# Performance work log

Measured on AMD Instinct MI355X. Metric: run time of the kernel, lower is better.

The kernel has to match this reference:

```python
import jax, jax.numpy as jnp
import numpy as np

C_IN, C_HID, N_HEADS = 128, 32, 4
INF = 1.0e9
LN_EPS = 1e-5


def setup_inputs() -> dict:
    key = jax.random.key(0)
    ks = jax.random.split(key, 12)
    B, I, J, C, H, D = 1, 384, 384, C_IN, N_HEADS, C_HID
    s = 0.02
    return {
        "x": jax.random.normal(ks[0], (B, I, J, C), dtype=jnp.float32),
        "mask": jnp.ones((B, I, J), dtype=jnp.float32),
        "ln_g": jnp.ones((C,), dtype=jnp.float32),
        "ln_b": jnp.zeros((C,), dtype=jnp.float32),
        "w_tri": jax.random.normal(ks[1], (C, H), dtype=jnp.float32) * s,
        "wq": jax.random.normal(ks[2], (C, H, D), dtype=jnp.float32) * s,
        "wk": jax.random.normal(ks[3], (C, H, D), dtype=jnp.float32) * s,
        "wv": jax.random.normal(ks[4], (C, H, D), dtype=jnp.float32) * s,
        "wg": jax.random.normal(ks[5], (C, H, D), dtype=jnp.float32) * s,
        "bg": jnp.ones((H, D), dtype=jnp.float32),
        "wo": jax.random.normal(ks[6], (H, D, C), dtype=jnp.float32) * s,
        "bo": jnp.zeros((C,), dtype=jnp.float32),
    }


def reference(x, mask, ln_g, ln_b, w_tri, wq, wk, wv, wg, bg, wo, bo):
    # LayerNorm over channel dim
    mu = jnp.mean(x, axis=-1, keepdims=True)
    var = jnp.mean(jnp.square(x - mu), axis=-1, keepdims=True)
    xn = (x - mu) * jax.lax.rsqrt(var + LN_EPS) * ln_g + ln_b  # [B,I,J,C]

    # mask bias: [B, I, 1, 1, J]
    mask_bias = (INF * (mask - 1.0))[..., :, None, None, :]
    # triangle bias: linear(x) -> [B,I,J,H] -> [B,1,H,I,J]
    tri_bias = jnp.einsum("bijc,ch->bhij", xn, w_tri)[:, None]

    scale = 1.0 / jnp.sqrt(jnp.asarray(C_HID, dtype=xn.dtype))
    # per-row attention over J: tensors [B, I, H, J, D]
    q = jnp.einsum("bixc,chd->bihxd", xn, wq) * scale
    k = jnp.einsum("bixc,chd->bihxd", xn, wk)
    v = jnp.einsum("bixc,chd->bihxd", xn, wv)

    logits = jnp.einsum("bihqd,bihkd->bihqk", q, k) + mask_bias + tri_bias
    a = jax.nn.softmax(logits, axis=-1)
    o = jnp.einsum("bihqk,bihkd->bihqd", a, v)  # [B,I,H,J,D]

    g = jax.nn.sigmoid(jnp.einsum("bixc,chd->bihxd", xn, wg) + bg[None, None, :, None, :])
    o = o * g
    out = jnp.einsum("bihxd,hdc->bixc", o, wo) + bo  # [B,I,J,C]
    return out
```

## Files before the change

kernel.cpp:

```cpp
#include <hip/hip_runtime.h>
#include <math.h>


#define I_DIM 384
#define J_DIM 384
#define C_DIM 128
#define H_DIM 4
#define D_DIM 32
#define NPOS (I_DIM * J_DIM)
#define Q_SCALE 0.17677669529663687f

typedef __attribute__((ext_vector_type(8))) short bf16x8;
typedef __attribute__((ext_vector_type(4))) float f32x4;

__device__ __forceinline__ float sigmoidf_(float v) {
    return 1.0f / (1.0f + __expf(-v));
}
__device__ __forceinline__ unsigned short f2bf(float f) {
    union { float f; unsigned u; } x; x.f = f;
    unsigned u = x.u;
    u += 0x7fffu + ((u >> 16) & 1u);
    return (unsigned short)(u >> 16);
}
__device__ __forceinline__ float bf2f(unsigned short v) {
    union { unsigned u; float f; } x; x.u = ((unsigned)v) << 16;
    return x.f;
}

__global__ __launch_bounds__(256) void prep_kernel(
    const float* __restrict__ wq, const float* __restrict__ wk,
    const float* __restrict__ wv, const float* __restrict__ wg,
    const float* __restrict__ wo, unsigned short* __restrict__ Wt)
{
    const int mat = blockIdx.x;
    const float* W = (mat == 0) ? wq : (mat == 1) ? wk : (mat == 2) ? wv
                    : (mat == 3) ? wg : wo;
    const float scale = (mat == 0) ? Q_SCALE : 1.0f;
    const int t = threadIdx.x;
    const int n = t >> 1, c0 = (t & 1) * 64;
#pragma unroll
    for (int u = 0; u < 8; ++u) {
        unsigned pk[4];
#pragma unroll
        for (int w = 0; w < 4; ++w) {
            const unsigned short a = f2bf(W[(size_t)(c0 + u * 8 + w * 2 + 0) * 128 + n] * scale);
            const unsigned short b = f2bf(W[(size_t)(c0 + u * 8 + w * 2 + 1) * 128 + n] * scale);
            pk[w] = (unsigned)a | ((unsigned)b << 16);
        }
        int4 q; q.x = pk[0]; q.y = pk[1]; q.z = pk[2]; q.w = pk[3];
        *(int4*)(Wt + (size_t)mat * 16384 + n * 128 + c0 + u * 8) = q;
    }
}

__global__ __launch_bounds__(256, 4) void proj_kernel(
    const float* __restrict__ x, const float* __restrict__ ln_g,
    const float* __restrict__ ln_b, const float* __restrict__ w_tri,
    const unsigned short* __restrict__ Wt, const float* __restrict__ bg,
    unsigned short* __restrict__ qb, unsigned short* __restrict__ kb,
    unsigned short* __restrict__ vb, unsigned short* __restrict__ gb,
    float* __restrict__ tri)
{
    __shared__ unsigned short At[128 * 128];
    __shared__ unsigned short Ct[128 * 32];

    const int t = threadIdx.x;
    const int pos0 = blockIdx.x * 128;
    const int lane = t & 63, wave = t >> 6;
    const int q15 = lane & 15, quad = lane >> 4;

    {
        const int g = t >> 2, q = t & 3;
#pragma unroll
        for (int rr = 0; rr < 2; ++rr) {
            const int r = g * 2 + rr;
            const float* xrow = x + (size_t)(pos0 + r) * C_DIM + q * 32;
            float xv[32];
            float s = 0.f, ss = 0.f;
#pragma unroll
            for (int u = 0; u < 8; ++u) {
                float4 v4 = ((const float4*)xrow)[u];
                xv[u * 4 + 0] = v4.x; xv[u * 4 + 1] = v4.y;
                xv[u * 4 + 2] = v4.z; xv[u * 4 + 3] = v4.w;
                s  += v4.x + v4.y + v4.z + v4.w;
                ss += v4.x * v4.x + v4.y * v4.y + v4.z * v4.z + v4.w * v4.w;
            }
            s  += __shfl_xor(s, 1);  s  += __shfl_xor(s, 2);
            ss += __shfl_xor(ss, 1); ss += __shfl_xor(ss, 2);
            const float mu  = s * (1.0f / 128.0f);
            const float var = ss * (1.0f / 128.0f) - mu * mu;
            const float rstd = rsqrtf(var + 1e-5f);

            float ptri[4] = {0.f, 0.f, 0.f, 0.f};
#pragma unroll
            for (int u2 = 0; u2 < 4; ++u2) {
                const int cb = q * 32 + u2 * 8;
                const float4 g0 = *(const float4*)(ln_g + cb);
                const float4 g1 = *(const float4*)(ln_g + cb + 4);
                const float4 b0 = *(const float4*)(ln_b + cb);
                const float4 b1 = *(const float4*)(ln_b + cb + 4);
                float xn8[8];
                xn8[0] = (xv[u2 * 8 + 0] - mu) * rstd * g0.x + b0.x;
                xn8[1] = (xv[u2 * 8 + 1] - mu) * rstd * g0.y + b0.y;
                xn8[2] = (xv[u2 * 8 + 2] - mu) * rstd * g0.z + b0.z;
                xn8[3] = (xv[u2 * 8 + 3] - mu) * rstd * g0.w + b0.w;
                xn8[4] = (xv[u2 * 8 + 4] - mu) * rstd * g1.x + b1.x;
                xn8[5] = (xv[u2 * 8 + 5] - mu) * rstd * g1.y + b1.y;
                xn8[6] = (xv[u2 * 8 + 6] - mu) * rstd * g1.z + b1.z;
                xn8[7] = (xv[u2 * 8 + 7] - mu) * rstd * g1.w + b1.w;
#pragma unroll
                for (int w = 0; w < 8; ++w) {
                    const float4 wt = ((const float4*)w_tri)[cb + w];
                    ptri[0] += xn8[w] * wt.x; ptri[1] += xn8[w] * wt.y;
                    ptri[2] += xn8[w] * wt.z; ptri[3] += xn8[w] * wt.w;
                }
                unsigned pk[4];
#pragma unroll
                for (int w = 0; w < 4; ++w)
                    pk[w] = (unsigned)f2bf(xn8[w * 2]) | ((unsigned)f2bf(xn8[w * 2 + 1]) << 16);
                int4 q4; q4.x = pk[0]; q4.y = pk[1]; q4.z = pk[2]; q4.w = pk[3];
                const int c = q * 4 + u2;
                *(int4*)&At[r * 128 + ((c ^ (r & 7)) * 8)] = q4;
            }
#pragma unroll
            for (int hh = 0; hh < 4; ++hh) {
                ptri[hh] += __shfl_xor(ptri[hh], 1);
                ptri[hh] += __shfl_xor(ptri[hh], 2);
            }
            const int pos = pos0 + r;
            const int i = pos / J_DIM, j = pos - (pos / J_DIM) * J_DIM;
            tri[((size_t)q * J_DIM + j) * I_DIM + i] = ptri[q];
        }
    }
    __syncthreads();

    const int m0 = wave * 32;
    for (int mat = 0; mat < 4; ++mat) {
        const unsigned short* WtM = Wt + (size_t)mat * 16384;

        f32x4 acc[2][8];
#pragma unroll
        for (int mt = 0; mt < 2; ++mt)
#pragma unroll
            for (int nt = 0; nt < 8; ++nt) acc[mt][nt] = (f32x4){0.f, 0.f, 0.f, 0.f};

#pragma unroll
        for (int kk = 0; kk < 4; ++kk) {
            const int sw = ((kk * 4 + quad) ^ (q15 & 7)) * 8;
            const bf16x8 a0 = *(const bf16x8*)&At[(m0 + q15) * 128 + sw];
            const bf16x8 a1 = *(const bf16x8*)&At[(m0 + 16 + q15) * 128 + sw];
            const unsigned short* bp = WtM + q15 * 128 + (kk * 4 + quad) * 8;
#pragma unroll
            for (int nt = 0; nt < 8; ++nt) {
                const bf16x8 b = *(const bf16x8*)(bp + nt * 16 * 128);
                acc[0][nt] = __builtin_amdgcn_mfma_f32_16x16x32_bf16(a0, b, acc[0][nt], 0, 0, 0);
                acc[1][nt] = __builtin_amdgcn_mfma_f32_16x16x32_bf16(a1, b, acc[1][nt], 0, 0, 0);
            }
        }

        unsigned short* O = (mat == 0) ? qb : (mat == 1) ? kb : (mat == 2) ? vb : gb;
#pragma unroll
        for (int qp = 0; qp < 4; ++qp) {
            __syncthreads();
#pragma unroll
            for (int mt = 0; mt < 2; ++mt)
#pragma unroll
                for (int n2 = 0; n2 < 2; ++n2) {
                    const int nt = qp * 2 + n2;
                    const int lc = n2 * 16 + q15;
                    const float bgl = (mat == 3) ? bg[qp * 32 + lc] : 0.f;
#pragma unroll
                    for (int reg = 0; reg < 4; ++reg) {
                        float v = acc[mt][nt][reg];
                        if (mat == 3) v = sigmoidf_(v + bgl);
                        const int row = m0 + mt * 16 + quad * 4 + reg;
                        const int cs = ((lc >> 3) ^ (row & 3) ^ ((row >> 2) & 3)) & 3;
                        Ct[row * 32 + cs * 8 + (lc & 7)] = f2bf(v);
                    }
                }
            __syncthreads();
#pragma unroll
            for (int s = 0; s < 2; ++s) {
                const int ch = s * 256 + t;
                const int r = ch >> 2, c = ch & 3;
                const int cs = (c ^ (r & 3) ^ ((r >> 2) & 3)) & 3;
                const int4 v = *(const int4*)&Ct[r * 32 + cs * 8];
                const int pos = pos0 + r;
                const int i = pos / J_DIM, j = pos - (pos / J_DIM) * J_DIM;
                *(int4*)(O + (((size_t)i * H_DIM + qp) * J_DIM + j) * D_DIM + c * 8) = v;
            }
        }
    }
}

__global__ __launch_bounds__(256) void attn_kernel(
    const unsigned short* __restrict__ qb, const unsigned short* __restrict__ kb,
    const unsigned short* __restrict__ vb, unsigned short* gob,
    const float* __restrict__ triT, const float* __restrict__ mask)
{
    __shared__ unsigned short Klds[64 * 32];
    __shared__ unsigned short Vt[32 * 68];
    __shared__ unsigned short Plds[4][32 * 68];
    __shared__ float Mb[J_DIM];

    const int t = threadIdx.x;
    const int lane = t & 63, wave = t >> 6;
    const int q15 = lane & 15, quad = lane >> 4;
    const int i = blockIdx.x >> 2, h = blockIdx.x & 3;
    const size_t hb = (size_t)(i * H_DIM + h) * (J_DIM * D_DIM);
    const int m0 = wave * 96;

    for (int idx = t; idx < J_DIM; idx += 256)
        Mb[idx] = 1.0e9f * (mask[i * J_DIM + idx] - 1.0f);

    bf16x8 qf[6];
#pragma unroll
    for (int m = 0; m < 6; ++m)
        qf[m] = *(const bf16x8*)(qb + hb + (size_t)(m0 + m * 16 + q15) * D_DIM + quad * 8);

    f32x4 Oacc[6][2];
    float sums[6][4];
#pragma unroll
    for (int m = 0; m < 6; ++m) {
#pragma unroll
        for (int d2 = 0; d2 < 2; ++d2) Oacc[m][d2] = (f32x4){0.f, 0.f, 0.f, 0.f};
#pragma unroll
        for (int r = 0; r < 4; ++r) sums[m][r] = 0.f;
    }

    unsigned short* Pw = Plds[wave];
    const float* triH = triT + (size_t)h * J_DIM * I_DIM;

    for (int kt = 0; kt < 6; ++kt) {
        __syncthreads();
        {
            const int kp = t >> 2, du = (t & 3) * 8;
            const size_t gsrc = hb + (size_t)(kt * 64 + kp) * D_DIM + du;
            *(int4*)&Klds[kp * 32 + du] = *(const int4*)(kb + gsrc);
            int4 vv = *(const int4*)(vb + gsrc);
            const unsigned short* vs = (const unsigned short*)&vv;
#pragma unroll
            for (int u = 0; u < 8; ++u)
                Vt[(du + u) * 68 + kp] = vs[u];
        }
        __syncthreads();

        bf16x8 vf[2][2];
#pragma unroll
        for (int ks = 0; ks < 2; ++ks)
#pragma unroll
            for (int d2 = 0; d2 < 2; ++d2)
                vf[ks][d2] = *(const bf16x8*)&Vt[(d2 * 16 + q15) * 68 + ks * 32 + quad * 8];

#pragma unroll
        for (int pass = 0; pass < 3; ++pass) {
            const int mbase = pass * 2;

#pragma unroll
            for (int nt = 0; nt < 4; ++nt) {
                const bf16x8 kf = *(const bf16x8*)&Klds[(nt * 16 + q15) * 32 + quad * 8];
                const float mb = Mb[kt * 64 + nt * 16 + q15];
                const float* tcol = triH + (size_t)(kt * 64 + nt * 16 + q15) * I_DIM;
#pragma unroll
                for (int mm = 0; mm < 2; ++mm) {
                    const int m = mbase + mm;
                    const float4 tb = *(const float4*)(tcol + m0 + m * 16 + quad * 4);
                    f32x4 s = {0.f, 0.f, 0.f, 0.f};
                    s = __builtin_amdgcn_mfma_f32_16x16x32_bf16(qf[m], kf, s, 0, 0, 0);
                    const float p0 = __expf(s[0] + mb + tb.x);
                    const float p1 = __expf(s[1] + mb + tb.y);
                    const float p2 = __expf(s[2] + mb + tb.z);
                    const float p3 = __expf(s[3] + mb + tb.w);
                    sums[m][0] += p0; sums[m][1] += p1;
                    sums[m][2] += p2; sums[m][3] += p3;
                    const int row = mm * 16 + quad * 4;
                    const int col = nt * 16 + q15;
                    Pw[(row + 0) * 68 + col] = f2bf(p0);
                    Pw[(row + 1) * 68 + col] = f2bf(p1);
                    Pw[(row + 2) * 68 + col] = f2bf(p2);
                    Pw[(row + 3) * 68 + col] = f2bf(p3);
                }
            }

#pragma unroll
            for (int mm = 0; mm < 2; ++mm) {
                const int m = mbase + mm;
#pragma unroll
                for (int ks = 0; ks < 2; ++ks) {
                    const bf16x8 af = *(const bf16x8*)&Pw[(mm * 16 + q15) * 68 + ks * 32 + quad * 8];
                    Oacc[m][0] = __builtin_amdgcn_mfma_f32_16x16x32_bf16(af, vf[ks][0], Oacc[m][0], 0, 0, 0);
                    Oacc[m][1] = __builtin_amdgcn_mfma_f32_16x16x32_bf16(af, vf[ks][1], Oacc[m][1], 0, 0, 0);
                }
            }
        }
    }

    float inv[6][4];
#pragma unroll
    for (int m = 0; m < 6; ++m)
#pragma unroll
        for (int r = 0; r < 4; ++r) {
            float s0 = sums[m][r];
            s0 += __shfl_xor(s0, 1); s0 += __shfl_xor(s0, 2);
            s0 += __shfl_xor(s0, 4); s0 += __shfl_xor(s0, 8);
            inv[m][r] = 1.0f / s0;
        }

#pragma unroll
    for (int m = 0; m < 6; ++m) {
        const int qrow = m0 + m * 16 + quad * 4;
#pragma unroll
        for (int d2 = 0; d2 < 2; ++d2) {
            const int d = d2 * 16 + q15;
#pragma unroll
            for (int r = 0; r < 4; ++r) {
                const size_t idx = hb + (size_t)(qrow + r) * D_DIM + d;
                const float g = bf2f(gob[idx]);
                gob[idx] = f2bf(Oacc[m][d2][r] * inv[m][r] * g);
            }
        }
    }
}

__global__ __launch_bounds__(256, 4) void out_kernel(
    const unsigned short* __restrict__ og, const unsigned short* __restrict__ WtO,
    const float* __restrict__ bo, float* __restrict__ out)
{
    __shared__ unsigned short At[128 * 128];

    const int t = threadIdx.x;
    const int pos0 = blockIdx.x * 128;
    const int lane = t & 63, wave = t >> 6;
    const int q15 = lane & 15, quad = lane >> 4;

    {
        const int r = t >> 1, half = t & 1;
        const int pos = pos0 + r;
        const int i = pos / J_DIM, j = pos - (pos / J_DIM) * J_DIM;
#pragma unroll
        for (int u = 0; u < 8; ++u) {
            const int k0 = half * 64 + u * 8;
            const int hh = k0 >> 5, d0 = k0 & 31;
            const int4 v = *(const int4*)(og + (((size_t)i * H_DIM + hh) * J_DIM + j) * D_DIM + d0);
            const int c = half * 8 + u;
            *(int4*)&At[r * 128 + ((c ^ (r & 7)) * 8)] = v;
        }
    }
    __syncthreads();

    const int m0 = wave * 32;
    f32x4 acc[2][8];
#pragma unroll
    for (int mt = 0; mt < 2; ++mt)
#pragma unroll
        for (int nt = 0; nt < 8; ++nt) acc[mt][nt] = (f32x4){0.f, 0.f, 0.f, 0.f};

#pragma unroll
    for (int kk = 0; kk < 4; ++kk) {
        const int sw = ((kk * 4 + quad) ^ (q15 & 7)) * 8;
        const bf16x8 a0 = *(const bf16x8*)&At[(m0 + q15) * 128 + sw];
        const bf16x8 a1 = *(const bf16x8*)&At[(m0 + 16 + q15) * 128 + sw];
        const unsigned short* bp = WtO + q15 * 128 + (kk * 4 + quad) * 8;
#pragma unroll
        for (int nt = 0; nt < 8; ++nt) {
            const bf16x8 b = *(const bf16x8*)(bp + nt * 16 * 128);
            acc[0][nt] = __builtin_amdgcn_mfma_f32_16x16x32_bf16(a0, b, acc[0][nt], 0, 0, 0);
            acc[1][nt] = __builtin_amdgcn_mfma_f32_16x16x32_bf16(a1, b, acc[1][nt], 0, 0, 0);
        }
    }

#pragma unroll
    for (int mt = 0; mt < 2; ++mt)
#pragma unroll
        for (int nt = 0; nt < 8; ++nt) {
            const float bov = bo[nt * 16 + q15];
#pragma unroll
            for (int reg = 0; reg < 4; ++reg) {
                const int pos = pos0 + m0 + mt * 16 + quad * 4 + reg;
                out[(size_t)pos * C_DIM + nt * 16 + q15] = acc[mt][nt][reg] + bov;
            }
        }
}

extern "C" void kernel_launch(void* const* d_in, const int* in_sizes, int n_in,
                              void* d_out, int out_size, void* d_ws, size_t ws_size,
                              hipStream_t stream)
{
    const float* x     = (const float*)d_in[0];
    const float* mask  = (const float*)d_in[1];
    const float* ln_g  = (const float*)d_in[2];
    const float* ln_b  = (const float*)d_in[3];
    const float* w_tri = (const float*)d_in[4];
    const float* wq    = (const float*)d_in[5];
    const float* wk    = (const float*)d_in[6];
    const float* wv    = (const float*)d_in[7];
    const float* wg    = (const float*)d_in[8];
    const float* bg    = (const float*)d_in[9];
    const float* wo    = (const float*)d_in[10];
    const float* bo    = (const float*)d_in[11];
    float* out = (float*)d_out;
    char* ws = (char*)d_ws;

    const size_t NE = (size_t)NPOS * 128;
    unsigned short* qb = (unsigned short*)ws;
    unsigned short* kb = (unsigned short*)(ws + NE * 2);
    unsigned short* vb = (unsigned short*)(ws + NE * 4);
    unsigned short* gb = (unsigned short*)(ws + NE * 6);
    float*         tri = (float*)(ws + NE * 8);
    unsigned short* Wt = (unsigned short*)(ws + NE * 8 + (size_t)NPOS * 4 * 4);

    prep_kernel<<<5, 256, 0, stream>>>(wq, wk, wv, wg, wo, Wt);
    proj_kernel<<<NPOS / 128, 256, 0, stream>>>(x, ln_g, ln_b, w_tri, Wt, bg,
                                                qb, kb, vb, gb, tri);
    attn_kernel<<<I_DIM * H_DIM, 256, 0, stream>>>(qb, kb, vb, gb, tri, mask);
    out_kernel<<<NPOS / 128, 256, 0, stream>>>(gb, Wt + 4 * 16384, bo, out);
}
```

Baseline: 537.8 us.

## Coalesce tri writes with separate transpose, widen proj epilogue, stage WtO in LDS

The projection kernel now writes the triangle bias in row-major [h][i][j] order, giving coalesced stores instead of strided transposed ones. A new in-place tile-transpose kernel then restores the [h][j][i] layout that attention expects. The proj epilogue stages the full 128-column tile in a larger LDS buffer with one sync pair per matrix instead of four, and out_kernel loads the output weight matrix into swizzled LDS rather than reading it from global memory per MFMA. The cost is an extra kernel launch and another pass over tri, plus more LDS per block (and occupancy hints removed), which may cut occupancy.

Result: slower. 564.5 us (+5.0%).

```diff
diff --git a/kernel.cpp b/kernel.cpp
--- a/kernel.cpp
+++ b/kernel.cpp
@@ -52,7 +52,7 @@
     }
 }
 
-__global__ __launch_bounds__(256, 4) void proj_kernel(
+__global__ __launch_bounds__(256) void proj_kernel(
     const float* __restrict__ x, const float* __restrict__ ln_g,
     const float* __restrict__ ln_b, const float* __restrict__ w_tri,
     const unsigned short* __restrict__ Wt, const float* __restrict__ bg,
@@ -61,7 +61,7 @@
     float* __restrict__ tri)
 {
     __shared__ unsigned short At[128 * 128];
-    __shared__ unsigned short Ct[128 * 32];
+    __shared__ unsigned short Ct[128 * 128];
 
     const int t = threadIdx.x;
     const int pos0 = blockIdx.x * 128;
@@ -128,7 +128,7 @@
             }
             const int pos = pos0 + r;
             const int i = pos / J_DIM, j = pos - (pos / J_DIM) * J_DIM;
-            tri[((size_t)q * J_DIM + j) * I_DIM + i] = ptri[q];
+            tri[((size_t)q * I_DIM + i) * J_DIM + j] = ptri[q];
         }
     }
     __syncthreads();
@@ -157,38 +157,70 @@
             }
         }
 
-        unsigned short* O = (mat == 0) ? qb : (mat == 1) ? kb : (mat == 2) ? vb : gb;
-#pragma unroll
-        for (int qp = 0; qp < 4; ++qp) {
-            __syncthreads();
-#pragma unroll
-            for (int mt = 0; mt < 2; ++mt)
-#pragma unroll
-                for (int n2 = 0; n2 < 2; ++n2) {
-                    const int nt = qp * 2 + n2;
-                    const int lc = n2 * 16 + q15;
-                    const float bgl = (mat == 3) ? bg[qp * 32 + lc] : 0.f;
-#pragma unroll
-                    for (int reg = 0; reg < 4; ++reg) {
-                        float v = acc[mt][nt][reg];
-                        if (mat == 3) v = sigmoidf_(v + bgl);
-                        const int row = m0 + mt * 16 + quad * 4 + reg;
-                        const int cs = ((lc >> 3) ^ (row & 3) ^ ((row >> 2) & 3)) & 3;
-                        Ct[row * 32 + cs * 8 + (lc & 7)] = f2bf(v);
-                    }
+        __syncthreads();
+#pragma unroll
+        for (int mt = 0; mt < 2; ++mt)
+#pragma unroll
+            for (int nt = 0; nt < 8; ++nt) {
+                const int col = nt * 16 + q15;
+                const float bgl = (mat == 3) ? bg[col] : 0.f;
+#pragma unroll
+                for (int reg = 0; reg < 4; ++reg) {
+                    float v = acc[mt][nt][reg];
+                    if (mat == 3) v = sigmoidf_(v + bgl);
+                    const int row = m0 + mt * 16 + quad * 4 + reg;
+                    Ct[row * 128 + (((col >> 3) ^ (row & 7)) * 8) + (col & 7)] = f2bf(v);
                 }
-            __syncthreads();
-#pragma unroll
-            for (int s = 0; s < 2; ++s) {
-                const int ch = s * 256 + t;
-                const int r = ch >> 2, c = ch & 3;
-                const int cs = (c ^ (r & 3) ^ ((r >> 2) & 3)) & 3;
-                const int4 v = *(const int4*)&Ct[r * 32 + cs * 8];
+            }
+        __syncthreads();
+        {
+            unsigned short* O = (mat == 0) ? qb : (mat == 1) ? kb : (mat == 2) ? vb : gb;
+#pragma unroll
+            for (int sgm = 0; sgm < 2; ++sgm) {
+                const int ch = t + sgm * 256;
+                const int r = ch >> 2, hh = ch & 3;
                 const int pos = pos0 + r;
                 const int i = pos / J_DIM, j = pos - (pos / J_DIM) * J_DIM;
-                *(int4*)(O + (((size_t)i * H_DIM + qp) * J_DIM + j) * D_DIM + c * 8) = v;
-            }
-        }
+                unsigned short* dst = O + (((size_t)i * H_DIM + hh) * J_DIM + j) * D_DIM;
+#pragma unroll
+                for (int w = 0; w < 4; ++w) {
+                    const int c = hh * 4 + w;
+                    *(int4*)(dst + w * 8) = *(const int4*)&Ct[r * 128 + ((c ^ (r & 7)) * 8)];
+                }
+            }
+        }
+    }
+}
+
+__global__ __launch_bounds__(256) void tri_tr_kernel(float* __restrict__ tri)
+{
+    const int h = blockIdx.x / 78;
+    int rem = blockIdx.x - h * 78;
+    int ti = 0;
+    while (rem >= 12 - ti) { rem -= 12 - ti; ++ti; }
+    const int tj = ti + rem;
+
+    float* T = tri + (size_t)h * I_DIM * J_DIM;
+    __shared__ float A[32][33];
+    __shared__ float B[32][33];
+
+    const int t = threadIdx.x;
+    const int r = t >> 3, c4 = (t & 7) * 4;
+
+    {
+        const float4 v = *(const float4*)(T + (size_t)(ti * 32 + r) * J_DIM + tj * 32 + c4);
+        A[r][c4 + 0] = v.x; A[r][c4 + 1] = v.y; A[r][c4 + 2] = v.z; A[r][c4 + 3] = v.w;
+        const float4 w = *(const float4*)(T + (size_t)(tj * 32 + r) * J_DIM + ti * 32 + c4);
+        B[r][c4 + 0] = w.x; B[r][c4 + 1] = w.y; B[r][c4 + 2] = w.z; B[r][c4 + 3] = w.w;
+    }
+    __syncthreads();
+    {
+        float4 v;
+        v.x = B[c4 + 0][r]; v.y = B[c4 + 1][r]; v.z = B[c4 + 2][r]; v.w = B[c4 + 3][r];
+        *(float4*)(T + (size_t)(ti * 32 + r) * J_DIM + tj * 32 + c4) = v;
+        float4 w;
+        w.x = A[c4 + 0][r]; w.y = A[c4 + 1][r]; w.z = A[c4 + 2][r]; w.w = A[c4 + 3][r];
+        *(float4*)(T + (size_t)(tj * 32 + r) * J_DIM + ti * 32 + c4) = w;
     }
 }
 
@@ -321,11 +353,12 @@
     }
 }
 
-__global__ __launch_bounds__(256, 4) void out_kernel(
+__global__ __launch_bounds__(256) void out_kernel(
     const unsigned short* __restrict__ og, const unsigned short* __restrict__ WtO,
     const float* __restrict__ bo, float* __restrict__ out)
 {
     __shared__ unsigned short At[128 * 128];
+    __shared__ unsigned short Bt[128 * 128];
 
     const int t = threadIdx.x;
     const int pos0 = blockIdx.x * 128;
@@ -344,6 +377,12 @@
             const int c = half * 8 + u;
             *(int4*)&At[r * 128 + ((c ^ (r & 7)) * 8)] = v;
         }
+        const unsigned short* src = WtO + r * 128 + half * 64;
+#pragma unroll
+        for (int u = 0; u < 8; ++u) {
+            const int c = half * 8 + u;
+            *(int4*)&Bt[r * 128 + ((c ^ (r & 7)) * 8)] = *(const int4*)(src + u * 8);
+        }
     }
     __syncthreads();
 
@@ -359,10 +398,9 @@
         const int sw = ((kk * 4 + quad) ^ (q15 & 7)) * 8;
         const bf16x8 a0 = *(const bf16x8*)&At[(m0 + q15) * 128 + sw];
         const bf16x8 a1 = *(const bf16x8*)&At[(m0 + 16 + q15) * 128 + sw];
-        const unsigned short* bp = WtO + q15 * 128 + (kk * 4 + quad) * 8;
 #pragma unroll
         for (int nt = 0; nt < 8; ++nt) {
-            const bf16x8 b = *(const bf16x8*)(bp + nt * 16 * 128);
+            const bf16x8 b = *(const bf16x8*)&Bt[(nt * 16 + q15) * 128 + sw];
             acc[0][nt] = __builtin_amdgcn_mfma_f32_16x16x32_bf16(a0, b, acc[0][nt], 0, 0, 0);
             acc[1][nt] = __builtin_amdgcn_mfma_f32_16x16x32_bf16(a1, b, acc[1][nt], 0, 0, 0);
         }
@@ -411,6 +449,7 @@
     prep_kernel<<<5, 256, 0, stream>>>(wq, wk, wv, wg, wo, Wt);
     proj_kernel<<<NPOS / 128, 256, 0, stream>>>(x, ln_g, ln_b, w_tri, Wt, bg,
                                                 qb, kb, vb, gb, tri);
+    tri_tr_kernel<<<H_DIM * 78, 256, 0, stream>>>(tri);
     attn_kernel<<<I_DIM * H_DIM, 256, 0, stream>>>(qb, kb, vb, gb, tri, mask);
     out_kernel<<<NPOS / 128, 256, 0, stream>>>(gb, Wt + 4 * 16384, bo, out);
 }
```

## Fuse attention with output projection; write tri bias coalesced then transpose in place

Applied to the files above, without the earlier changes.

The attention and output-projection kernels are merged. Each block handles one row i and half of the queries, with one wave per head. The gated attention output is staged in LDS and multiplied by Wo directly, so the intermediate gated tensor is no longer written to and read back from global memory. The projection kernel now stores the triangle bias in coalesced [h,i,j] order, and a new in-place 32x32 tile transpose kernel converts it to the [h,j,i] layout the attention kernel expects. In exchange, each wave loads its own K/V tiles (more LDS and more global traffic per block), there are fewer blocks per head, and the output GEMM is split unevenly across waves.

After: 756.6 us. +40.7%, slower.

```diff
diff --git a/kernel.cpp b/kernel.cpp
--- a/kernel.cpp
+++ b/kernel.cpp
@@ -128,7 +128,7 @@
             }
             const int pos = pos0 + r;
             const int i = pos / J_DIM, j = pos - (pos / J_DIM) * J_DIM;
-            tri[((size_t)q * J_DIM + j) * I_DIM + i] = ptri[q];
+            tri[((size_t)q * I_DIM + i) * J_DIM + j] = ptri[q];
         }
     }
     __syncthreads();
@@ -192,193 +192,222 @@
     }
 }
 
-__global__ __launch_bounds__(256) void attn_kernel(
+__global__ __launch_bounds__(256) void tri_tr_kernel(float* __restrict__ tri)
+{
+    const int h = blockIdx.x / 78;
+    int rem = blockIdx.x - h * 78;
+    int ti = 0;
+    while (rem >= 12 - ti) { rem -= 12 - ti; ++ti; }
+    const int tj = ti + rem;
+
+    float* T = tri + (size_t)h * I_DIM * J_DIM;
+    __shared__ float A[32][33];
+    __shared__ float B[32][33];
+
+    const int t = threadIdx.x;
+    const int r = t >> 3, c4 = (t & 7) * 4;
+
+    {
+        const float4 v = *(const float4*)(T + (size_t)(ti * 32 + r) * J_DIM + tj * 32 + c4);
+        A[r][c4 + 0] = v.x; A[r][c4 + 1] = v.y; A[r][c4 + 2] = v.z; A[r][c4 + 3] = v.w;
+        const float4 w = *(const float4*)(T + (size_t)(tj * 32 + r) * J_DIM + ti * 32 + c4);
+        B[r][c4 + 0] = w.x; B[r][c4 + 1] = w.y; B[r][c4 + 2] = w.z; B[r][c4 + 3] = w.w;
+    }
+    __syncthreads();
+    {
+        float4 v;
+        v.x = B[c4 + 0][r]; v.y = B[c4 + 1][r]; v.z = B[c4 + 2][r]; v.w = B[c4 + 3][r];
+        *(float4*)(T + (size_t)(ti * 32 + r) * J_DIM + tj * 32 + c4) = v;
+        float4 w;
+        w.x = A[c4 + 0][r]; w.y = A[c4 + 1][r]; w.z = A[c4 + 2][r]; w.w = A[c4 + 3][r];
+        *(float4*)(T + (size_t)(tj * 32 + r) * J_DIM + ti * 32 + c4) = w;
+    }
+}
+
+struct SmemKVP {
+    unsigned short K[4][64 * 32];
+    unsigned short V[4][32 * 68];
+    unsigned short P[4][32 * 68];
+};
+union SmemU {
+    SmemKVP a;
+    unsigned short og[96 * 128];
+};
+
+__global__ __launch_bounds__(256, 3) void attn_out_kernel(
     const unsigned short* __restrict__ qb, const unsigned short* __restrict__ kb,
-    const unsigned short* __restrict__ vb, unsigned short* gob,
-    const float* __restrict__ triT, const float* __restrict__ mask)
+    const unsigned short* __restrict__ vb, const unsigned short* __restrict__ gb,
+    const float* __restrict__ triT, const float* __restrict__ mask,
+    const unsigned short* __restrict__ WtO, const float* __restrict__ bo,
+    float* __restrict__ out)
 {
-    __shared__ unsigned short Klds[64 * 32];
-    __shared__ unsigned short Vt[32 * 68];
-    __shared__ unsigned short Plds[4][32 * 68];
+    __shared__ SmemU sm;
     __shared__ float Mb[J_DIM];
 
     const int t = threadIdx.x;
     const int lane = t & 63, wave = t >> 6;
     const int q15 = lane & 15, quad = lane >> 4;
-    const int i = blockIdx.x >> 2, h = blockIdx.x & 3;
+    const int i = blockIdx.x >> 1, half = blockIdx.x & 1;
+    const int h = wave;
     const size_t hb = (size_t)(i * H_DIM + h) * (J_DIM * D_DIM);
-    const int m0 = wave * 96;
+    const float* triH = triT + (size_t)h * J_DIM * I_DIM;
 
     for (int idx = t; idx < J_DIM; idx += 256)
         Mb[idx] = 1.0e9f * (mask[i * J_DIM + idx] - 1.0f);
 
-    bf16x8 qf[6];
-#pragma unroll
-    for (int m = 0; m < 6; ++m)
-        qf[m] = *(const bf16x8*)(qb + hb + (size_t)(m0 + m * 16 + q15) * D_DIM + quad * 8);
-
-    f32x4 Oacc[6][2];
-    float sums[6][4];
-#pragma unroll
-    for (int m = 0; m < 6; ++m) {
-#pragma unroll
-        for (int d2 = 0; d2 < 2; ++d2) Oacc[m][d2] = (f32x4){0.f, 0.f, 0.f, 0.f};
-#pragma unroll
-        for (int r = 0; r < 4; ++r) sums[m][r] = 0.f;
-    }
-
-    unsigned short* Pw = Plds[wave];
-    const float* triH = triT + (size_t)h * J_DIM * I_DIM;
-
-    for (int kt = 0; kt < 6; ++kt) {
+    unsigned short* Kw = sm.a.K[wave];
+    unsigned short* Vw = sm.a.V[wave];
+    unsigned short* Pw = sm.a.P[wave];
+
+    for (int sub = 0; sub < 2; ++sub) {
+        const int q0 = half * 192 + sub * 96;
         __syncthreads();
-        {
-            const int kp = t >> 2, du = (t & 3) * 8;
-            const size_t gsrc = hb + (size_t)(kt * 64 + kp) * D_DIM + du;
-            *(int4*)&Klds[kp * 32 + du] = *(const int4*)(kb + gsrc);
-            int4 vv = *(const int4*)(vb + gsrc);
-            const unsigned short* vs = (const unsigned short*)&vv;
-#pragma unroll
-            for (int u = 0; u < 8; ++u)
-                Vt[(du + u) * 68 + kp] = vs[u];
-        }
-        __syncthreads();
-
-        bf16x8 vf[2][2];
-#pragma unroll
-        for (int ks = 0; ks < 2; ++ks)
-#pragma unroll
-            for (int d2 = 0; d2 < 2; ++d2)
-                vf[ks][d2] = *(const bf16x8*)&Vt[(d2 * 16 + q15) * 68 + ks * 32 + quad * 8];
-
-#pragma unroll
-        for (int pass = 0; pass < 3; ++pass) {
-            const int mbase = pass * 2;
-
-#pragma unroll
-            for (int nt = 0; nt < 4; ++nt) {
-                const bf16x8 kf = *(const bf16x8*)&Klds[(nt * 16 + q15) * 32 + quad * 8];
-                const float mb = Mb[kt * 64 + nt * 16 + q15];
-                const float* tcol = triH + (size_t)(kt * 64 + nt * 16 + q15) * I_DIM;
+
+        bf16x8 qf[6];
+#pragma unroll
+        for (int m = 0; m < 6; ++m)
+            qf[m] = *(const bf16x8*)(qb + hb + (size_t)(q0 + m * 16 + q15) * D_DIM + quad * 8);
+
+        f32x4 Oacc[6][2];
+        float sums[6][4];
+#pragma unroll
+        for (int m = 0; m < 6; ++m) {
+#pragma unroll
+            for (int d2 = 0; d2 < 2; ++d2) Oacc[m][d2] = (f32x4){0.f, 0.f, 0.f, 0.f};
+#pragma unroll
+            for (int r = 0; r < 4; ++r) sums[m][r] = 0.f;
+        }
+
+        for (int kt = 0; kt < 6; ++kt) {
+            {
+                const size_t gsrc = hb + (size_t)(kt * 64 + lane) * D_DIM;
+                int4 k0 = *(const int4*)(kb + gsrc);
+                int4 k1 = *(const int4*)(kb + gsrc + 8);
+                int4 k2 = *(const int4*)(kb + gsrc + 16);
+                int4 k3 = *(const int4*)(kb + gsrc + 24);
+                *(int4*)&Kw[lane * 32 + 0]  = k0;
+                *(int4*)&Kw[lane * 32 + 8]  = k1;
+                *(int4*)&Kw[lane * 32 + 16] = k2;
+                *(int4*)&Kw[lane * 32 + 24] = k3;
+                int4 vv[4];
+                vv[0] = *(const int4*)(vb + gsrc);
+                vv[1] = *(const int4*)(vb + gsrc + 8);
+                vv[2] = *(const int4*)(vb + gsrc + 16);
+                vv[3] = *(const int4*)(vb + gsrc + 24);
+#pragma unroll
+                for (int p = 0; p < 4; ++p) {
+                    const unsigned short* vs = (const unsigned short*)&vv[p];
+#pragma unroll
+                    for (int u = 0; u < 8; ++u)
+                        Vw[(p * 8 + u) * 68 + lane] = vs[u];
+                }
+            }
+
+            bf16x8 vf[2][2];
+#pragma unroll
+            for (int ks = 0; ks < 2; ++ks)
+#pragma unroll
+                for (int d2 = 0; d2 < 2; ++d2)
+                    vf[ks][d2] = *(const bf16x8*)&Vw[(d2 * 16 + q15) * 68 + ks * 32 + quad * 8];
+
+#pragma unroll
+            for (int pass = 0; pass < 3; ++pass) {
+                const int mbase = pass * 2;
+#pragma unroll
+                for (int nt = 0; nt < 4; ++nt) {
+                    const bf16x8 kf = *(const bf16x8*)&Kw[(nt * 16 + q15) * 32 + quad * 8];
+                    const float mb = Mb[kt * 64 + nt * 16 + q15];
+                    const float* tcol = triH + (size_t)(kt * 64 + nt * 16 + q15) * I_DIM;
+#pragma unroll
+                    for (int mm = 0; mm < 2; ++mm) {
+                        const int m = mbase + mm;
+                        const float4 tb = *(const float4*)(tcol + q0 + m * 16 + quad * 4);
+                        f32x4 s = {0.f, 0.f, 0.f, 0.f};
+                        s = __builtin_amdgcn_mfma_f32_16x16x32_bf16(qf[m], kf, s, 0, 0, 0);
+                        const float p0 = __expf(s[0] + mb + tb.x);
+                        const float p1 = __expf(s[1] + mb + tb.y);
+                        const float p2 = __expf(s[2] + mb + tb.z);
+                        const float p3 = __expf(s[3] + mb + tb.w);
+                        sums[m][0] += p0; sums[m][1] += p1;
+                        sums[m][2] += p2; sums[m][3] += p3;
+                        const int row = mm * 16 + quad * 4;
+                        const int col = nt * 16 + q15;
+                        Pw[(row + 0) * 68 + col] = f2bf(p0);
+                        Pw[(row + 1) * 68 + col] = f2bf(p1);
+                        Pw[(row + 2) * 68 + col] = f2bf(p2);
+                        Pw[(row + 3) * 68 + col] = f2bf(p3);
+                    }
+                }
 #pragma unroll
                 for (int mm = 0; mm < 2; ++mm) {
                     const int m = mbase + mm;
-                    const float4 tb = *(const float4*)(tcol + m0 + m * 16 + quad * 4);
-                    f32x4 s = {0.f, 0.f, 0.f, 0.f};
-                    s = __builtin_amdgcn_mfma_f32_16x16x32_bf16(qf[m], kf, s, 0, 0, 0);
-                    const float p0 = __expf(s[0] + mb + tb.x);
-                    const float p1 = __expf(s[1] + mb + tb.y);
-                    const float p2 = __expf(s[2] + mb + tb.z);
-                    const float p3 = __expf(s[3] + mb + tb.w);
-                    sums[m][0] += p0; sums[m][1] += p1;
-                    sums[m][2] += p2; sums[m][3] += p3;
-                    const int row = mm * 16 + quad * 4;
-                    const int col = nt * 16 + q15;
-                    Pw[(row + 0) * 68 + col] = f2bf(p0);
-                    Pw[(row + 1) * 68 + col] = f2bf(p1);
-                    Pw[(row + 2) * 68 + col] = f2bf(p2);
-                    Pw[(row + 3) * 68 + col] = f2bf(p3);
-                }
-            }
-
-#pragma unroll
-            for (int mm = 0; mm < 2; ++mm) {
-                const int m = mbase + mm;
-#pragma unroll
-                for (int ks = 0; ks < 2; ++ks) {
-                    const bf16x8 af = *(const bf16x8*)&Pw[(mm * 16 + q15) * 68 + ks * 32 + quad * 8];
-                    Oacc[m][0] = __builtin_amdgcn_mfma_f32_16x16x32_bf16(af, vf[ks][0], Oacc[m][0], 0, 0, 0);
-                    Oacc[m][1] = __builtin_amdgcn_mfma_f32_16x16x32_bf16(af, vf[ks][1], Oacc[m][1], 0, 0, 0);
-                }
-            }
-        }
-    }
-
-    float inv[6][4];
-#pragma unroll
-    for (int m = 0; m < 6; ++m)
-#pragma unroll
-        for (int r = 0; r < 4; ++r) {
-            float s0 = sums[m][r];
-            s0 += __shfl_xor(s0, 1); s0 += __shfl_xor(s0, 2);
-            s0 += __shfl_xor(s0, 4); s0 += __shfl_xor(s0, 8);
-            inv[m][r] = 1.0f / s0;
-        }
-
-#pragma unroll
-    for (int m = 0; m < 6; ++m) {
-        const int qrow = m0 + m * 16 + quad * 4;
-#pragma unroll
-        for (int d2 = 0; d2 < 2; ++d2) {
-            const int d = d2 * 16 + q15;
+#pragma unroll
+                    for (int ks = 0; ks < 2; ++ks) {
+                        const bf16x8 af = *(const bf16x8*)&Pw[(mm * 16 + q15) * 68 + ks * 32 + quad * 8];
+                        Oacc[m][0] = __builtin_amdgcn_mfma_f32_16x16x32_bf16(af, vf[ks][0], Oacc[m][0], 0, 0, 0);
+                        Oacc[m][1] = __builtin_amdgcn_mfma_f32_16x16x32_bf16(af, vf[ks][1], Oacc[m][1], 0, 0, 0);
+                    }
+                }
+            }
+        }
+
+        float inv[6][4];
+#pragma unroll
+        for (int m = 0; m < 6; ++m)
 #pragma unroll
             for (int r = 0; r < 4; ++r) {
-                const size_t idx = hb + (size_t)(qrow + r) * D_DIM + d;
-                const float g = bf2f(gob[idx]);
-                gob[idx] = f2bf(Oacc[m][d2][r] * inv[m][r] * g);
-            }
-        }
-    }
-}
-
-__global__ __launch_bounds__(256, 4) void out_kernel(
-    const unsigned short* __restrict__ og, const unsigned short* __restrict__ WtO,
-    const float* __restrict__ bo, float* __restrict__ out)
-{
-    __shared__ unsigned short At[128 * 128];
-
-    const int t = threadIdx.x;
-    const int pos0 = blockIdx.x * 128;
-    const int lane = t & 63, wave = t >> 6;
-    const int q15 = lane & 15, quad = lane >> 4;
-
-    {
-        const int r = t >> 1, half = t & 1;
-        const int pos = pos0 + r;
-        const int i = pos / J_DIM, j = pos - (pos / J_DIM) * J_DIM;
-#pragma unroll
-        for (int u = 0; u < 8; ++u) {
-            const int k0 = half * 64 + u * 8;
-            const int hh = k0 >> 5, d0 = k0 & 31;
-            const int4 v = *(const int4*)(og + (((size_t)i * H_DIM + hh) * J_DIM + j) * D_DIM + d0);
-            const int c = half * 8 + u;
-            *(int4*)&At[r * 128 + ((c ^ (r & 7)) * 8)] = v;
-        }
-    }
-    __syncthreads();
-
-    const int m0 = wave * 32;
-    f32x4 acc[2][8];
-#pragma unroll
-    for (int mt = 0; mt < 2; ++mt)
-#pragma unroll
-        for (int nt = 0; nt < 8; ++nt) acc[mt][nt] = (f32x4){0.f, 0.f, 0.f, 0.f};
-
-#pragma unroll
-    for (int kk = 0; kk < 4; ++kk) {
-        const int sw = ((kk * 4 + quad) ^ (q15 & 7)) * 8;
-        const bf16x8 a0 = *(const bf16x8*)&At[(m0 + q15) * 128 + sw];
-        const bf16x8 a1 = *(const bf16x8*)&At[(m0 + 16 + q15) * 128 + sw];
-        const unsigned short* bp = WtO + q15 * 128 + (kk * 4 + quad) * 8;
-#pragma unroll
-        for (int nt = 0; nt < 8; ++nt) {
-            const bf16x8 b = *(const bf16x8*)(bp + nt * 16 * 128);
-            acc[0][nt] = __builtin_amdgcn_mfma_f32_16x16x32_bf16(a0, b, acc[0][nt], 0, 0, 0);
-            acc[1][nt] = __builtin_amdgcn_mfma_f32_16x16x32_bf16(a1, b, acc[1][nt], 0, 0, 0);
-        }
-    }
-
-#pragma unroll
-    for (int mt = 0; mt < 2; ++mt)
-#pragma unroll
-        for (int nt = 0; nt < 8; ++nt) {
-            const float bov = bo[nt * 16 + q15];
-#pragma unroll
-            for (int reg = 0; reg < 4; ++reg) {
-                const int pos = pos0 + m0 + mt * 16 + quad * 4 + reg;
-                out[(size_t)pos * C_DIM + nt * 16 + q15] = acc[mt][nt][reg] + bov;
-            }
-        }
+                float s0 = sums[m][r];
+                s0 += __shfl_xor(s0, 1); s0 += __shfl_xor(s0, 2);
+                s0 += __shfl_xor(s0, 4); s0 += __shfl_xor(s0, 8);
+                inv[m][r] = 1.0f / s0;
+            }
+
+        __syncthreads();
+#pragma unroll
+        for (int m = 0; m < 6; ++m) {
+#pragma unroll
+            for (int d2 = 0; d2 < 2; ++d2) {
+                const int d = d2 * 16 + q15;
+                const int col = h * 32 + d;
+#pragma unroll
+                for (int reg = 0; reg < 4; ++reg) {
+                    const int row = m * 16 + quad * 4 + reg;
+                    const float g = bf2f(gb[hb + (size_t)(q0 + row) * D_DIM + d]);
+                    const float o = Oacc[m][d2][reg] * inv[m][reg] * g;
+                    sm.og[row * 128 + (((col >> 3) ^ (row & 7)) * 8) + (col & 7)] = f2bf(o);
+                }
+            }
+        }
+        __syncthreads();
+
+        const int mtb = (wave < 2) ? wave * 2 : (wave + 2);
+        const int mte = (wave < 2) ? mtb + 2 : mtb + 1;
+        for (int mt = mtb; mt < mte; ++mt) {
+            f32x4 acc[8];
+#pragma unroll
+            for (int nt = 0; nt < 8; ++nt) acc[nt] = (f32x4){0.f, 0.f, 0.f, 0.f};
+#pragma unroll
+            for (int kk = 0; kk < 4; ++kk) {
+                const int sw = ((kk * 4 + quad) ^ (q15 & 7)) * 8;
+                const bf16x8 a = *(const bf16x8*)&sm.og[(mt * 16 + q15) * 128 + sw];
+                const unsigned short* bp = WtO + q15 * 128 + (kk * 4 + quad) * 8;
+#pragma unroll
+                for (int nt = 0; nt < 8; ++nt) {
+                    const bf16x8 b = *(const bf16x8*)(bp + nt * 16 * 128);
+                    acc[nt] = __builtin_amdgcn_mfma_f32_16x16x32_bf16(a, b, acc[nt], 0, 0, 0);
+                }
+            }
+#pragma unroll
+            for (int nt = 0; nt < 8; ++nt) {
+                const float bov = bo[nt * 16 + q15];
+#pragma unroll
+                for (int reg = 0; reg < 4; ++reg) {
+                    const int row = q0 + mt * 16 + quad * 4 + reg;
+                    out[(size_t)(i * J_DIM + row) * C_DIM + nt * 16 + q15] = acc[nt][reg] + bov;
+                }
+            }
+        }
+    }
 }
 
 extern "C" void kernel_launch(void* const* d_in, const int* in_sizes, int n_in,
@@ -411,6 +440,7 @@
     prep_kernel<<<5, 256, 0, stream>>>(wq, wk, wv, wg, wo, Wt);
     proj_kernel<<<NPOS / 128, 256, 0, stream>>>(x, ln_g, ln_b, w_tri, Wt, bg,
                                                 qb, kb, vb, gb, tri);
-    attn_kernel<<<I_DIM * H_DIM, 256, 0, stream>>>(qb, kb, vb, gb, tri, mask);
-    out_kernel<<<NPOS / 128, 256, 0, stream>>>(gb, Wt + 4 * 16384, bo, out);
-}
+    tri_tr_kernel<<<H_DIM * 78, 256, 0, stream>>>(tri);
+    attn_out_kernel<<<I_DIM * 2, 256, 0, stream>>>(qb, kb, vb, gb, tri, mask,
+                                                   Wt + 4 * 16384, bo, out);
+}
```
